# Optimization experiments

Measured on AMD Instinct MI355X. Metric: run time of the kernel, lower is better.

The kernel has to match this reference:

```python
import jax, jax.numpy as jnp
import numpy as np

N_EMBED = 1024
HEAD_SIZE = 128
B, T = 8, 2048


def setup_inputs() -> dict:
    key = jax.random.key(0)
    kx, kk, kq, kv = jax.random.split(key, 4)
    x = jax.random.normal(kx, (B, T, N_EMBED), dtype=jnp.float32)
    Wk = jax.random.normal(kk, (N_EMBED, HEAD_SIZE), dtype=jnp.float32) * (N_EMBED ** -0.5)
    Wq = jax.random.normal(kq, (N_EMBED, HEAD_SIZE), dtype=jnp.float32) * (N_EMBED ** -0.5)
    Wv = jax.random.normal(kv, (N_EMBED, HEAD_SIZE), dtype=jnp.float32) * (N_EMBED ** -0.5)
    return {"x": x, "Wk": Wk, "Wq": Wq, "Wv": Wv}


def reference(x, Wk, Wq, Wv):
    # x: [B, T, C]; single-head causal attention, dropout rate 0 (identity)
    t = x.shape[1]
    k = jnp.einsum("btc,ch->bth", x, Wk)  # keys
    q = jnp.einsum("btc,ch->bth", x, Wq)  # queries
    v = jnp.einsum("btc,ch->bth", x, Wv)  # values
    scale = k.shape[-1] ** -0.5
    scores = jnp.einsum("bqh,bkh->bqk", q, k) * scale  # [B, T, T]
    causal = jnp.tril(jnp.ones((t, t), dtype=bool))
    scores = jnp.where(causal, scores, -jnp.inf)
    attn = jax.nn.softmax(scores, axis=-1)
    return jnp.einsum("bqk,bkh->bqh", attn, v)
```

## Files before the change

kernel.cpp:

```cpp
#include <hip/hip_runtime.h>
#include <hip/hip_bf16.h>
#include <math.h>

#define B_ 8
#define T_ 2048
#define C_ 1024
#define D_ 128
#define M_ (B_*T_)

typedef __attribute__((ext_vector_type(8))) short short8;
typedef __attribute__((ext_vector_type(4))) float floatx4;
typedef __hip_bfloat16 bf16;

#define QSCALE 0.12751744416218247f

__global__ __launch_bounds__(256) void cvt_w2_kernel(const float* __restrict__ Wq,
                                                     const float* __restrict__ Wk,
                                                     const float* __restrict__ Wv,
                                                     bf16* __restrict__ Wt) {
    __shared__ bf16 tl[64][136];
    const int t = threadIdx.x;
    const int k0 = blockIdx.x * 64, g = blockIdx.y;
    const float* W = (g == 0) ? Wq : (g == 1) ? Wk : Wv;
    {
        int k = t >> 2, n0 = (t & 3) * 32;
        const float* src = W + (size_t)(k0 + k) * 128 + n0;
#pragma unroll
        for (int j = 0; j < 4; ++j) {
            float4 v0 = *(const float4*)(src + j * 8);
            float4 v1 = *(const float4*)(src + j * 8 + 4);
            union { short8 s; __hip_bfloat162 h[4]; } u;
            __hip_bfloat162 h;
            h.x = __float2bfloat16(v0.x); h.y = __float2bfloat16(v0.y); u.h[0] = h;
            h.x = __float2bfloat16(v0.z); h.y = __float2bfloat16(v0.w); u.h[1] = h;
            h.x = __float2bfloat16(v1.x); h.y = __float2bfloat16(v1.y); u.h[2] = h;
            h.x = __float2bfloat16(v1.z); h.y = __float2bfloat16(v1.w); u.h[3] = h;
            *(short8*)&tl[k][n0 + j * 8] = u.s;
        }
    }
    __syncthreads();
    {
        int n = t >> 1, ko = (t & 1) * 32;
        union { short8 s[4]; bf16 e[32]; } u;
#pragma unroll
        for (int i = 0; i < 32; ++i) u.e[i] = tl[ko + i][n];
        bf16* dst = Wt + (size_t)g * 131072 + (size_t)n * 1024 + k0 + ko;
#pragma unroll
        for (int j = 0; j < 4; ++j) *(short8*)(dst + j * 8) = u.s[j];
    }
}

__global__ __launch_bounds__(512, 2) void proj5_kernel(const float* __restrict__ x,
                                                       const bf16* __restrict__ Wt,
                                                       bf16* __restrict__ Qb,
                                                       bf16* __restrict__ Kb,
                                                       bf16* __restrict__ Vt) {
    __shared__ bf16 la[64][72];
    __shared__ bf16 lb[384][72];
    const int t = threadIdx.x;
    const int wave = t >> 6, lane = t & 63;
    const int quad = lane >> 4, l15 = lane & 15;
    const int wr2 = wave >> 2, wc2 = wave & 3;
    const int row0 = blockIdx.x * 64;
    const int ar = t >> 3, ao = (t & 7) * 8;

    floatx4 acc[2][6];
#pragma unroll
    for (int m = 0; m < 2; ++m)
#pragma unroll
        for (int n = 0; n < 6; ++n) acc[m][n] = (floatx4)0.0f;

    float4 xr0, xr1;
    short8 wreg[6];
    {
        const float* src = x + (size_t)(row0 + ar) * 1024 + ao;
        xr0 = *(const float4*)src;
        xr1 = *(const float4*)(src + 4);
#pragma unroll
        for (int j = 0; j < 6; ++j) {
            int c = t + j * 512;
            int rb = c >> 3, ob = (c & 7) * 8;
            wreg[j] = *(const short8*)(Wt + (size_t)rb * 1024 + ob);
        }
    }

    for (int kc = 0; kc < 16; ++kc) {
        __syncthreads();
        {
            union { short8 s; __hip_bfloat162 h[4]; } u;
            __hip_bfloat162 h;
            h.x = __float2bfloat16(xr0.x); h.y = __float2bfloat16(xr0.y); u.h[0] = h;
            h.x = __float2bfloat16(xr0.z); h.y = __float2bfloat16(xr0.w); u.h[1] = h;
            h.x = __float2bfloat16(xr1.x); h.y = __float2bfloat16(xr1.y); u.h[2] = h;
            h.x = __float2bfloat16(xr1.z); h.y = __float2bfloat16(xr1.w); u.h[3] = h;
            *(short8*)&la[ar][ao] = u.s;
        }
#pragma unroll
        for (int j = 0; j < 6; ++j) {
            int c = t + j * 512;
            int rb = c >> 3, ob = (c & 7) * 8;
            *(short8*)&lb[rb][ob] = wreg[j];
        }
        if (kc < 15) {
            const float* src = x + (size_t)(row0 + ar) * 1024 + (kc + 1) * 64 + ao;
            xr0 = *(const float4*)src;
            xr1 = *(const float4*)(src + 4);
#pragma unroll
            for (int j = 0; j < 6; ++j) {
                int c = t + j * 512;
                int rb = c >> 3, ob = (c & 7) * 8;
                wreg[j] = *(const short8*)(Wt + (size_t)rb * 1024 + (kc + 1) * 64 + ob);
            }
        }
        __syncthreads();
#pragma unroll
        for (int dk = 0; dk < 2; ++dk) {
            short8 af[2], bff[6];
#pragma unroll
            for (int m = 0; m < 2; ++m) af[m] = *(const short8*)&la[wr2 * 32 + m * 16 + l15][dk * 32 + quad * 8];
#pragma unroll
            for (int n = 0; n < 6; ++n) bff[n] = *(const short8*)&lb[wc2 * 96 + n * 16 + l15][dk * 32 + quad * 8];
#pragma unroll
            for (int m = 0; m < 2; ++m)
#pragma unroll
                for (int n = 0; n < 6; ++n)
                    acc[m][n] = __builtin_amdgcn_mfma_f32_16x16x32_bf16(af[m], bff[n], acc[m][n], 0, 0, 0);
        }
    }

    __syncthreads();
    bf16* vtl = &lb[0][0];
#pragma unroll
    for (int m = 0; m < 2; ++m)
#pragma unroll
        for (int r = 0; r < 4; ++r) {
            const int tt = wr2 * 32 + m * 16 + quad * 4 + r;
            const int row = row0 + tt;
#pragma unroll
            for (int n = 0; n < 6; ++n) {
                const int colb = wc2 * 96 + n * 16;
                const int g = colb >> 7;
                const int lc = (colb & 127) + l15;
                const float v = acc[m][n][r];
                if (g == 0)      Qb[(size_t)row * 128 + lc] = __float2bfloat16(v * QSCALE);
                else if (g == 1) Kb[(size_t)row * 128 + lc] = __float2bfloat16(v);
                else             vtl[tt * 136 + lc] = __float2bfloat16(v);
            }
        }
    __syncthreads();
    {
        int d = t >> 2, toff = (t & 3) * 16;
        union { short8 s[2]; bf16 e[16]; } u;
#pragma unroll
        for (int i = 0; i < 16; ++i) u.e[i] = vtl[(toff + i) * 136 + d];
        int bb = row0 >> 11, t0 = row0 & 2047;
        bf16* dst = Vt + (size_t)(bb * D_ + d) * T_ + t0 + toff;
        *(short8*)(dst)     = u.s[0];
        *(short8*)(dst + 8) = u.s[1];
    }
}

__global__ __launch_bounds__(256, 3) void flash_fm2_kernel(const bf16* __restrict__ Qb,
                                                           const bf16* __restrict__ Kb,
                                                           const bf16* __restrict__ Vt,
                                                           float* __restrict__ out,
                                                           bf16* __restrict__ Opart,
                                                           float* __restrict__ Lpart) {
    const int tile = blockIdx.x, seg = blockIdx.y, b = blockIdx.z;
    const int keys_total = (tile + 1) * 64;
    const int nseg = (keys_total + 255) >> 8;
    if (seg >= nseg) return;

    __shared__ bf16 lds_k[64][136];
    __shared__ bf16 lds_v[128][72];
    __shared__ bf16 lds_p[4][16][72];
    const int t = threadIdx.x;
    const int wave = t >> 6, lane = t & 63;
    const int quad = lane >> 4, l15 = lane & 15;
    const int q0 = tile * 64;
    const int k_start = seg << 8;
    const int k_end = min(k_start + 256, keys_total);
    const int nch = (k_end - k_start) >> 6;

    short8 qf[4];
    {
        int qm = q0 + wave * 16 + l15;
#pragma unroll
        for (int dk = 0; dk < 4; ++dk)
            qf[dk] = *(const short8*)(Qb + (size_t)(b * T_ + qm) * 128 + dk * 32 + quad * 8);
    }

    short8 kreg[4], vreg[4];
    {
        const int k0 = k_start;
#pragma unroll
        for (int j = 0; j < 4; ++j) {
            int c = t + j * 256;
            { int r = c >> 4, co = (c & 15) * 8;
              kreg[j] = *(const short8*)(Kb + (size_t)(b * T_ + k0 + r) * 128 + co); }
            { int d = c >> 3, co = (c & 7) * 8;
              vreg[j] = *(const short8*)(Vt + (size_t)b * (D_ * T_) + d * T_ + k0 + co); }
        }
    }

    floatx4 o_acc[8];
#pragma unroll
    for (int i = 0; i < 8; ++i) o_acc[i] = (floatx4)0.0f;
    float lp[4] = {0.f, 0.f, 0.f, 0.f};
    const int qrow = q0 + wave * 16 + quad * 4;

    for (int ch = 0; ch < nch; ++ch) {
        const int k0 = k_start + (ch << 6);
        __syncthreads();
#pragma unroll
        for (int j = 0; j < 4; ++j) {
            int c = t + j * 256;
            { int r = c >> 4, co = (c & 15) * 8; *(short8*)&lds_k[r][co] = kreg[j]; }
            { int d = c >> 3, co = (c & 7) * 8;  *(short8*)&lds_v[d][co] = vreg[j]; }
        }
        if (ch + 1 < nch) {
            const int kn = k0 + 64;
#pragma unroll
            for (int j = 0; j < 4; ++j) {
                int c = t + j * 256;
                { int r = c >> 4, co = (c & 15) * 8;
                  kreg[j] = *(const short8*)(Kb + (size_t)(b * T_ + kn + r) * 128 + co); }
                { int d = c >> 3, co = (c & 7) * 8;
                  vreg[j] = *(const short8*)(Vt + (size_t)b * (D_ * T_) + d * T_ + kn + co); }
            }
        }
        __syncthreads();

        floatx4 s[4];
#pragma unroll
        for (int nt = 0; nt < 4; ++nt) s[nt] = (floatx4)0.0f;
#pragma unroll
        for (int dk = 0; dk < 4; ++dk)
#pragma unroll
            for (int nt = 0; nt < 4; ++nt) {
                short8 kb = *(const short8*)&lds_k[nt * 16 + l15][dk * 32 + quad * 8];
                s[nt] = __builtin_amdgcn_mfma_f32_16x16x32_bf16(qf[dk], kb, s[nt], 0, 0, 0);
            }

        float sv[4][4];
#pragma unroll
        for (int nt = 0; nt < 4; ++nt)
#pragma unroll
            for (int r = 0; r < 4; ++r) sv[nt][r] = s[nt][r];

        if (k0 + 63 > q0) {
#pragma unroll
            for (int nt = 0; nt < 4; ++nt) {
                int key = k0 + nt * 16 + l15;
#pragma unroll
                for (int r = 0; r < 4; ++r)
                    if (key > qrow + r) sv[nt][r] = -1e30f;
            }
        }

#pragma unroll
        for (int nt = 0; nt < 4; ++nt)
#pragma unroll
            for (int r = 0; r < 4; ++r) sv[nt][r] = exp2f(sv[nt][r]);
#pragma unroll
        for (int r = 0; r < 4; ++r)
            lp[r] += (sv[0][r] + sv[1][r]) + (sv[2][r] + sv[3][r]);

#pragma unroll
        for (int nt = 0; nt < 4; ++nt)
#pragma unroll
            for (int r = 0; r < 4; ++r)
                lds_p[wave][quad * 4 + r][nt * 16 + l15] = __float2bfloat16(sv[nt][r]);
        short8 pa0 = *(const short8*)&lds_p[wave][l15][quad * 8];
        short8 pa1 = *(const short8*)&lds_p[wave][l15][32 + quad * 8];

#pragma unroll
        for (int nt = 0; nt < 8; ++nt) {
            short8 vb0 = *(const short8*)&lds_v[nt * 16 + l15][quad * 8];
            short8 vb1 = *(const short8*)&lds_v[nt * 16 + l15][32 + quad * 8];
            o_acc[nt] = __builtin_amdgcn_mfma_f32_16x16x32_bf16(pa0, vb0, o_acc[nt], 0, 0, 0);
            o_acc[nt] = __builtin_amdgcn_mfma_f32_16x16x32_bf16(pa1, vb1, o_acc[nt], 0, 0, 0);
        }
    }

    float l_i[4];
#pragma unroll
    for (int r = 0; r < 4; ++r) {
        float v = lp[r];
        v += __shfl_xor(v, 1);
        v += __shfl_xor(v, 2);
        v += __shfl_xor(v, 4);
        v += __shfl_xor(v, 8);
        l_i[r] = v;
    }

    const int lrow = wave * 16 + quad * 4;
    if (nseg == 1) {
        float inv_l[4];
#pragma unroll
        for (int r = 0; r < 4; ++r) inv_l[r] = 1.0f / l_i[r];
#pragma unroll
        for (int f = 0; f < 8; ++f)
#pragma unroll
            for (int r = 0; r < 4; ++r)
                out[(size_t)(b * T_ + qrow + r) * 128 + f * 16 + l15] = o_acc[f][r] * inv_l[r];
    } else {
        int pre = 0;
        for (int u = 4; u < tile; ++u) pre += (u + 4) >> 2;
        const size_t slot = (size_t)b * 140 + pre + seg;
        bf16* ob = Opart + slot * (64 * 128);
#pragma unroll
        for (int f = 0; f < 8; ++f)
#pragma unroll
            for (int r = 0; r < 4; ++r)
                ob[(size_t)(lrow + r) * 128 + f * 16 + l15] = __float2bfloat16(o_acc[f][r]);
        if (l15 == 0) {
#pragma unroll
            for (int r = 0; r < 4; ++r)
                Lpart[slot * 64 + lrow + r] = l_i[r];
        }
    }
}

__global__ __launch_bounds__(256) void combine4_kernel(const bf16* __restrict__ Opart,
                                                       const float* __restrict__ Lpart,
                                                       float* __restrict__ out) {
    const int tile = blockIdx.x + 4, b = blockIdx.y;
    const int nseg = (tile + 4) >> 2;
    int pre = 0;
    for (int u = 4; u < tile; ++u) pre += (u + 4) >> 2;
    const size_t slot0 = (size_t)b * 140 + pre;
    const int t = threadIdx.x;
    const int row = t >> 2, c0 = (t & 3) * 32;

    float lsum = 0.f;
    for (int j = 0; j < nseg; ++j) lsum += Lpart[(slot0 + j) * 64 + row];

    float acc[32];
#pragma unroll
    for (int i = 0; i < 32; ++i) acc[i] = 0.f;
    for (int j = 0; j < nseg; ++j) {
        const bf16* src = Opart + (slot0 + j) * (64 * 128) + (size_t)row * 128 + c0;
#pragma unroll
        for (int u = 0; u < 4; ++u) {
            short8 v8 = *(const short8*)(src + u * 8);
#pragma unroll
            for (int e = 0; e < 8; ++e) {
                union { unsigned int u32; float f; } cv;
                cv.u32 = ((unsigned int)(unsigned short)v8[e]) << 16;
                acc[u * 8 + e] += cv.f;
            }
        }
    }
    float inv = 1.0f / lsum;
    float* dst = out + (size_t)(b * T_ + tile * 64 + row) * 128 + c0;
#pragma unroll
    for (int i = 0; i < 32; ++i) dst[i] = acc[i] * inv;
}

extern "C" void kernel_launch(void* const* d_in, const int* in_sizes, int n_in,
                              void* d_out, int out_size, void* d_ws, size_t ws_size,
                              hipStream_t stream) {
    const float* x  = (const float*)d_in[0];
    const float* Wk = (const float*)d_in[1];
    const float* Wq = (const float*)d_in[2];
    const float* Wv = (const float*)d_in[3];
    float* out = (float*)d_out;

    char* ws = (char*)d_ws;
    bf16*  Wt    = (bf16*)ws;
    bf16*  Qb    = (bf16*)(ws + 786432);
    bf16*  Kb    = (bf16*)(ws + 4980736);
    bf16*  Vt    = (bf16*)(ws + 9175040);
    bf16*  Opart = (bf16*)(ws + 13369344);
    float* Lpart = (float*)(ws + 31719424);

    cvt_w2_kernel<<<dim3(16, 3), 256, 0, stream>>>(Wq, Wk, Wv, Wt);
    proj5_kernel<<<256, 512, 0, stream>>>(x, Wt, Qb, Kb, Vt);
    flash_fm2_kernel<<<dim3(32, 8, B_), 256, 0, stream>>>(Qb, Kb, Vt, out, Opart, Lpart);
    combine4_kernel<<<dim3(28, B_), 256, 0, stream>>>(Opart, Lpart, out);
}
```

Measured before the change: 82.16 us.

## Load projection MFMA operands directly from global memory, bypassing LDS staging

The projection kernel no longer stages x and W tiles through shared memory. Each lane loads its MFMA fragments straight from global memory into registers: x is prefetched one chunk ahead, and the weight fragments are loaded just before use. This removes two barriers per k-step and the LDS round trip, but it adds redundant global and L2 traffic, since the four waves that share x rows and the two waves that share W columns each fetch their own copy. The V transpose buffer also gets a 137 padding stride to reduce bank conflicts.

```diff
diff --git a/kernel.cpp b/kernel.cpp
--- a/kernel.cpp
+++ b/kernel.cpp
@@ -50,19 +50,20 @@
     }
 }
 
-__global__ __launch_bounds__(512, 2) void proj5_kernel(const float* __restrict__ x,
+__global__ __launch_bounds__(512, 2) void proj9_kernel(const float* __restrict__ x,
                                                        const bf16* __restrict__ Wt,
                                                        bf16* __restrict__ Qb,
                                                        bf16* __restrict__ Kb,
                                                        bf16* __restrict__ Vt) {
-    __shared__ bf16 la[64][72];
-    __shared__ bf16 lb[384][72];
+    __shared__ bf16 vtl[64 * 137];
     const int t = threadIdx.x;
     const int wave = t >> 6, lane = t & 63;
     const int quad = lane >> 4, l15 = lane & 15;
     const int wr2 = wave >> 2, wc2 = wave & 3;
     const int row0 = blockIdx.x * 64;
-    const int ar = t >> 3, ao = (t & 7) * 8;
+
+    const float* xb = x + (size_t)(row0 + wr2 * 32 + l15) * 1024 + quad * 8;
+    const bf16*  wb = Wt + (size_t)(wc2 * 96 + l15) * 1024 + quad * 8;
 
     floatx4 acc[2][6];
 #pragma unroll
@@ -70,66 +71,57 @@
 #pragma unroll
         for (int n = 0; n < 6; ++n) acc[m][n] = (floatx4)0.0f;
 
-    float4 xr0, xr1;
-    short8 wreg[6];
-    {
-        const float* src = x + (size_t)(row0 + ar) * 1024 + ao;
-        xr0 = *(const float4*)src;
-        xr1 = *(const float4*)(src + 4);
-#pragma unroll
-        for (int j = 0; j < 6; ++j) {
-            int c = t + j * 512;
-            int rb = c >> 3, ob = (c & 7) * 8;
-            wreg[j] = *(const short8*)(Wt + (size_t)rb * 1024 + ob);
-        }
-    }
+    float4 xp[8];
+#pragma unroll
+    for (int m = 0; m < 2; ++m)
+#pragma unroll
+        for (int dk = 0; dk < 2; ++dk) {
+            const float* s = xb + (size_t)m * 16384 + dk * 32;
+            xp[m * 4 + dk * 2 + 0] = *(const float4*)s;
+            xp[m * 4 + dk * 2 + 1] = *(const float4*)(s + 4);
+        }
 
     for (int kc = 0; kc < 16; ++kc) {
-        __syncthreads();
+        short8 af[2][2];
+#pragma unroll
+        for (int m = 0; m < 2; ++m)
+#pragma unroll
+            for (int dk = 0; dk < 2; ++dk) {
+                float4 a0 = xp[m * 4 + dk * 2 + 0];
+                float4 a1 = xp[m * 4 + dk * 2 + 1];
+                union { short8 s; __hip_bfloat162 h[4]; } u;
+                __hip_bfloat162 h;
+                h.x = __float2bfloat16(a0.x); h.y = __float2bfloat16(a0.y); u.h[0] = h;
+                h.x = __float2bfloat16(a0.z); h.y = __float2bfloat16(a0.w); u.h[1] = h;
+                h.x = __float2bfloat16(a1.x); h.y = __float2bfloat16(a1.y); u.h[2] = h;
+                h.x = __float2bfloat16(a1.z); h.y = __float2bfloat16(a1.w); u.h[3] = h;
+                af[m][dk] = u.s;
+            }
         {
-            union { short8 s; __hip_bfloat162 h[4]; } u;
-            __hip_bfloat162 h;
-            h.x = __float2bfloat16(xr0.x); h.y = __float2bfloat16(xr0.y); u.h[0] = h;
-            h.x = __float2bfloat16(xr0.z); h.y = __float2bfloat16(xr0.w); u.h[1] = h;
-            h.x = __float2bfloat16(xr1.x); h.y = __float2bfloat16(xr1.y); u.h[2] = h;
-            h.x = __float2bfloat16(xr1.z); h.y = __float2bfloat16(xr1.w); u.h[3] = h;
-            *(short8*)&la[ar][ao] = u.s;
-        }
-#pragma unroll
-        for (int j = 0; j < 6; ++j) {
-            int c = t + j * 512;
-            int rb = c >> 3, ob = (c & 7) * 8;
-            *(short8*)&lb[rb][ob] = wreg[j];
-        }
-        if (kc < 15) {
-            const float* src = x + (size_t)(row0 + ar) * 1024 + (kc + 1) * 64 + ao;
-            xr0 = *(const float4*)src;
-            xr1 = *(const float4*)(src + 4);
-#pragma unroll
-            for (int j = 0; j < 6; ++j) {
-                int c = t + j * 512;
-                int rb = c >> 3, ob = (c & 7) * 8;
-                wreg[j] = *(const short8*)(Wt + (size_t)rb * 1024 + (kc + 1) * 64 + ob);
-            }
-        }
-        __syncthreads();
+            const int kn = (kc + 1) & 15;
+#pragma unroll
+            for (int m = 0; m < 2; ++m)
+#pragma unroll
+                for (int dk = 0; dk < 2; ++dk) {
+                    const float* s = xb + (size_t)m * 16384 + kn * 64 + dk * 32;
+                    xp[m * 4 + dk * 2 + 0] = *(const float4*)s;
+                    xp[m * 4 + dk * 2 + 1] = *(const float4*)(s + 4);
+                }
+        }
 #pragma unroll
         for (int dk = 0; dk < 2; ++dk) {
-            short8 af[2], bff[6];
-#pragma unroll
-            for (int m = 0; m < 2; ++m) af[m] = *(const short8*)&la[wr2 * 32 + m * 16 + l15][dk * 32 + quad * 8];
-#pragma unroll
-            for (int n = 0; n < 6; ++n) bff[n] = *(const short8*)&lb[wc2 * 96 + n * 16 + l15][dk * 32 + quad * 8];
+            short8 bff[6];
+#pragma unroll
+            for (int n = 0; n < 6; ++n)
+                bff[n] = *(const short8*)(wb + (size_t)n * 16384 + kc * 64 + dk * 32);
 #pragma unroll
             for (int m = 0; m < 2; ++m)
 #pragma unroll
                 for (int n = 0; n < 6; ++n)
-                    acc[m][n] = __builtin_amdgcn_mfma_f32_16x16x32_bf16(af[m], bff[n], acc[m][n], 0, 0, 0);
-        }
-    }
-
-    __syncthreads();
-    bf16* vtl = &lb[0][0];
+                    acc[m][n] = __builtin_amdgcn_mfma_f32_16x16x32_bf16(af[m][dk], bff[n], acc[m][n], 0, 0, 0);
+        }
+    }
+
 #pragma unroll
     for (int m = 0; m < 2; ++m)
 #pragma unroll
@@ -144,7 +136,7 @@
                 const float v = acc[m][n][r];
                 if (g == 0)      Qb[(size_t)row * 128 + lc] = __float2bfloat16(v * QSCALE);
                 else if (g == 1) Kb[(size_t)row * 128 + lc] = __float2bfloat16(v);
-                else             vtl[tt * 136 + lc] = __float2bfloat16(v);
+                else             vtl[tt * 137 + lc] = __float2bfloat16(v);
             }
         }
     __syncthreads();
@@ -152,10 +144,10 @@
         int d = t >> 2, toff = (t & 3) * 16;
         union { short8 s[2]; bf16 e[16]; } u;
 #pragma unroll
-        for (int i = 0; i < 16; ++i) u.e[i] = vtl[(toff + i) * 136 + d];
+        for (int i = 0; i < 16; ++i) u.e[i] = vtl[(toff + i) * 137 + d];
         int bb = row0 >> 11, t0 = row0 & 2047;
         bf16* dst = Vt + (size_t)(bb * D_ + d) * T_ + t0 + toff;
-        *(short8*)(dst)     = u.s[0];
+        *(short8*)dst       = u.s[0];
         *(short8*)(dst + 8) = u.s[1];
     }
 }
@@ -376,7 +368,7 @@
     float* Lpart = (float*)(ws + 31719424);
 
     cvt_w2_kernel<<<dim3(16, 3), 256, 0, stream>>>(Wq, Wk, Wv, Wt);
-    proj5_kernel<<<256, 512, 0, stream>>>(x, Wt, Qb, Kb, Vt);
+    proj9_kernel<<<256, 512, 0, stream>>>(x, Wt, Qb, Kb, Vt);
     flash_fm2_kernel<<<dim3(32, 8, B_), 256, 0, stream>>>(Qb, Kb, Vt, out, Opart, Lpart);
     combine4_kernel<<<dim3(28, B_), 256, 0, stream>>>(Opart, Lpart, out);
 }
```

After: 132.3 us. 1.61x slower.

## Pre-swizzle weights into MFMA fragment order and stream them from registers

Applied to the files above, without the earlier changes.

The weight conversion kernel now writes W directly in MFMA B-fragment order, so the projection kernel loads B operands straight from global memory into registers and no longer stages them through LDS. Only the x tile goes through LDS, now double-buffered, which drops one barrier per k-step. Each wave computes a 64x48 output slice instead of 32x96, and the V transpose buffer uses a stride of 137 to reduce bank conflicts. The cost is more global loads per wave with less reuse of A, plus reliance on L2 for the weight fragments.

```diff
diff --git a/kernel.cpp b/kernel.cpp
--- a/kernel.cpp
+++ b/kernel.cpp
@@ -14,13 +14,14 @@
 
 #define QSCALE 0.12751744416218247f
 
-__global__ __launch_bounds__(256) void cvt_w2_kernel(const float* __restrict__ Wq,
+__global__ __launch_bounds__(256) void cvt_w3_kernel(const float* __restrict__ Wq,
                                                      const float* __restrict__ Wk,
                                                      const float* __restrict__ Wv,
-                                                     bf16* __restrict__ Wt) {
+                                                     bf16* __restrict__ Wt2) {
     __shared__ bf16 tl[64][136];
     const int t = threadIdx.x;
-    const int k0 = blockIdx.x * 64, g = blockIdx.y;
+    const int kc = blockIdx.x, g = blockIdx.y;
+    const int k0 = kc * 64;
     const float* W = (g == 0) ? Wq : (g == 1) ? Wk : Wv;
     {
         int k = t >> 2, n0 = (t & 3) * 32;
@@ -40,111 +41,121 @@
     }
     __syncthreads();
     {
-        int n = t >> 1, ko = (t & 1) * 32;
-        union { short8 s[4]; bf16 e[32]; } u;
-#pragma unroll
-        for (int i = 0; i < 32; ++i) u.e[i] = tl[ko + i][n];
-        bf16* dst = Wt + (size_t)g * 131072 + (size_t)n * 1024 + k0 + ko;
-#pragma unroll
-        for (int j = 0; j < 4; ++j) *(short8*)(dst + j * 8) = u.s[j];
-    }
-}
-
-__global__ __launch_bounds__(512, 2) void proj5_kernel(const float* __restrict__ x,
-                                                       const bf16* __restrict__ Wt,
-                                                       bf16* __restrict__ Qb,
-                                                       bf16* __restrict__ Kb,
-                                                       bf16* __restrict__ Vt) {
-    __shared__ bf16 la[64][72];
-    __shared__ bf16 lb[384][72];
+#pragma unroll
+        for (int j = 0; j < 4; ++j) {
+            int cid = t + j * 256;
+            int lane = cid & 63, dk = (cid >> 6) & 1, cb = cid >> 7;
+            int krow = dk * 32 + (lane >> 4) * 8;
+            int ncol = cb * 16 + (lane & 15);
+            union { short8 s; bf16 e[8]; } u;
+#pragma unroll
+            for (int e = 0; e < 8; ++e) u.e[e] = tl[krow + e][ncol];
+            bf16* dst = Wt2 + ((((size_t)(g * 8 + cb) * 16 + kc) * 2 + dk) * 64 + lane) * 8;
+            *(short8*)dst = u.s;
+        }
+    }
+}
+
+__global__ __launch_bounds__(512, 2) void proj10_kernel(const float* __restrict__ x,
+                                                        const bf16* __restrict__ Wt2,
+                                                        bf16* __restrict__ Qb,
+                                                        bf16* __restrict__ Kb,
+                                                        bf16* __restrict__ Vt) {
+    __shared__ bf16 smem[2 * 64 * 72];
     const int t = threadIdx.x;
     const int wave = t >> 6, lane = t & 63;
     const int quad = lane >> 4, l15 = lane & 15;
-    const int wr2 = wave >> 2, wc2 = wave & 3;
     const int row0 = blockIdx.x * 64;
-    const int ar = t >> 3, ao = (t & 7) * 8;
-
-    floatx4 acc[2][6];
-#pragma unroll
-    for (int m = 0; m < 2; ++m)
-#pragma unroll
-        for (int n = 0; n < 6; ++n) acc[m][n] = (floatx4)0.0f;
+    const int xrow = t >> 3, xc8 = (t & 7) * 8;
+    const float* xbase = x + (size_t)(row0 + xrow) * 1024 + xc8;
+    const bf16* wbase = Wt2 + (size_t)lane * 8;
+
+    floatx4 acc[4][3];
+#pragma unroll
+    for (int m = 0; m < 4; ++m)
+#pragma unroll
+        for (int n = 0; n < 3; ++n) acc[m][n] = (floatx4)0.0f;
 
     float4 xr0, xr1;
-    short8 wreg[6];
-    {
-        const float* src = x + (size_t)(row0 + ar) * 1024 + ao;
-        xr0 = *(const float4*)src;
-        xr1 = *(const float4*)(src + 4);
-#pragma unroll
-        for (int j = 0; j < 6; ++j) {
-            int c = t + j * 512;
-            int rb = c >> 3, ob = (c & 7) * 8;
-            wreg[j] = *(const short8*)(Wt + (size_t)rb * 1024 + ob);
-        }
-    }
+    short8 br[6];
+
+    xr0 = *(const float4*)xbase;
+    xr1 = *(const float4*)(xbase + 4);
+    {
+        union { short8 s; __hip_bfloat162 h[4]; } u;
+        __hip_bfloat162 h;
+        h.x = __float2bfloat16(xr0.x); h.y = __float2bfloat16(xr0.y); u.h[0] = h;
+        h.x = __float2bfloat16(xr0.z); h.y = __float2bfloat16(xr0.w); u.h[1] = h;
+        h.x = __float2bfloat16(xr1.x); h.y = __float2bfloat16(xr1.y); u.h[2] = h;
+        h.x = __float2bfloat16(xr1.z); h.y = __float2bfloat16(xr1.w); u.h[3] = h;
+        *(short8*)&smem[xrow * 72 + xc8] = u.s;
+    }
+    xr0 = *(const float4*)(xbase + 64);
+    xr1 = *(const float4*)(xbase + 68);
+#pragma unroll
+    for (int n = 0; n < 3; ++n)
+#pragma unroll
+        for (int dk = 0; dk < 2; ++dk)
+            br[dk * 3 + n] = *(const short8*)(wbase + ((size_t)((wave * 3 + n) * 16 + 0) * 1024 + dk * 512));
 
     for (int kc = 0; kc < 16; ++kc) {
         __syncthreads();
-        {
+        short8 brn[6];
+        if (kc < 15) {
+#pragma unroll
+            for (int n = 0; n < 3; ++n)
+#pragma unroll
+                for (int dk = 0; dk < 2; ++dk)
+                    brn[dk * 3 + n] = *(const short8*)(wbase + ((size_t)((wave * 3 + n) * 16 + kc + 1) * 1024 + dk * 512));
             union { short8 s; __hip_bfloat162 h[4]; } u;
             __hip_bfloat162 h;
             h.x = __float2bfloat16(xr0.x); h.y = __float2bfloat16(xr0.y); u.h[0] = h;
             h.x = __float2bfloat16(xr0.z); h.y = __float2bfloat16(xr0.w); u.h[1] = h;
             h.x = __float2bfloat16(xr1.x); h.y = __float2bfloat16(xr1.y); u.h[2] = h;
             h.x = __float2bfloat16(xr1.z); h.y = __float2bfloat16(xr1.w); u.h[3] = h;
-            *(short8*)&la[ar][ao] = u.s;
-        }
-#pragma unroll
-        for (int j = 0; j < 6; ++j) {
-            int c = t + j * 512;
-            int rb = c >> 3, ob = (c & 7) * 8;
-            *(short8*)&lb[rb][ob] = wreg[j];
+            *(short8*)&smem[((kc + 1) & 1) * 4608 + xrow * 72 + xc8] = u.s;
+        }
+        if (kc < 14) {
+            const float* s = xbase + (kc + 2) * 64;
+            xr0 = *(const float4*)s;
+            xr1 = *(const float4*)(s + 4);
+        }
+        const bf16* lc = smem + (kc & 1) * 4608;
+#pragma unroll
+        for (int dk = 0; dk < 2; ++dk) {
+            short8 af[4];
+#pragma unroll
+            for (int m = 0; m < 4; ++m)
+                af[m] = *(const short8*)&lc[(m * 16 + l15) * 72 + dk * 32 + quad * 8];
+#pragma unroll
+            for (int m = 0; m < 4; ++m)
+#pragma unroll
+                for (int n = 0; n < 3; ++n)
+                    acc[m][n] = __builtin_amdgcn_mfma_f32_16x16x32_bf16(af[m], br[dk * 3 + n], acc[m][n], 0, 0, 0);
         }
         if (kc < 15) {
-            const float* src = x + (size_t)(row0 + ar) * 1024 + (kc + 1) * 64 + ao;
-            xr0 = *(const float4*)src;
-            xr1 = *(const float4*)(src + 4);
-#pragma unroll
-            for (int j = 0; j < 6; ++j) {
-                int c = t + j * 512;
-                int rb = c >> 3, ob = (c & 7) * 8;
-                wreg[j] = *(const short8*)(Wt + (size_t)rb * 1024 + (kc + 1) * 64 + ob);
-            }
-        }
-        __syncthreads();
-#pragma unroll
-        for (int dk = 0; dk < 2; ++dk) {
-            short8 af[2], bff[6];
-#pragma unroll
-            for (int m = 0; m < 2; ++m) af[m] = *(const short8*)&la[wr2 * 32 + m * 16 + l15][dk * 32 + quad * 8];
-#pragma unroll
-            for (int n = 0; n < 6; ++n) bff[n] = *(const short8*)&lb[wc2 * 96 + n * 16 + l15][dk * 32 + quad * 8];
-#pragma unroll
-            for (int m = 0; m < 2; ++m)
-#pragma unroll
-                for (int n = 0; n < 6; ++n)
-                    acc[m][n] = __builtin_amdgcn_mfma_f32_16x16x32_bf16(af[m], bff[n], acc[m][n], 0, 0, 0);
+#pragma unroll
+            for (int i = 0; i < 6; ++i) br[i] = brn[i];
         }
     }
 
     __syncthreads();
-    bf16* vtl = &lb[0][0];
-#pragma unroll
-    for (int m = 0; m < 2; ++m)
+    bf16* vtl = smem;
+#pragma unroll
+    for (int m = 0; m < 4; ++m)
 #pragma unroll
         for (int r = 0; r < 4; ++r) {
-            const int tt = wr2 * 32 + m * 16 + quad * 4 + r;
+            const int tt = m * 16 + quad * 4 + r;
             const int row = row0 + tt;
 #pragma unroll
-            for (int n = 0; n < 6; ++n) {
-                const int colb = wc2 * 96 + n * 16;
+            for (int n = 0; n < 3; ++n) {
+                const int colb = wave * 48 + n * 16;
                 const int g = colb >> 7;
-                const int lc = (colb & 127) + l15;
+                const int lc_ = (colb & 127) + l15;
                 const float v = acc[m][n][r];
-                if (g == 0)      Qb[(size_t)row * 128 + lc] = __float2bfloat16(v * QSCALE);
-                else if (g == 1) Kb[(size_t)row * 128 + lc] = __float2bfloat16(v);
-                else             vtl[tt * 136 + lc] = __float2bfloat16(v);
+                if (g == 0)      Qb[(size_t)row * 128 + lc_] = __float2bfloat16(v * QSCALE);
+                else if (g == 1) Kb[(size_t)row * 128 + lc_] = __float2bfloat16(v);
+                else             vtl[tt * 137 + lc_] = __float2bfloat16(v);
             }
         }
     __syncthreads();
@@ -152,10 +163,10 @@
         int d = t >> 2, toff = (t & 3) * 16;
         union { short8 s[2]; bf16 e[16]; } u;
 #pragma unroll
-        for (int i = 0; i < 16; ++i) u.e[i] = vtl[(toff + i) * 136 + d];
+        for (int i = 0; i < 16; ++i) u.e[i] = vtl[(toff + i) * 137 + d];
         int bb = row0 >> 11, t0 = row0 & 2047;
         bf16* dst = Vt + (size_t)(bb * D_ + d) * T_ + t0 + toff;
-        *(short8*)(dst)     = u.s[0];
+        *(short8*)dst       = u.s[0];
         *(short8*)(dst + 8) = u.s[1];
     }
 }
@@ -368,15 +379,15 @@
     float* out = (float*)d_out;
 
     char* ws = (char*)d_ws;
-    bf16*  Wt    = (bf16*)ws;
+    bf16*  Wt2   = (bf16*)ws;
     bf16*  Qb    = (bf16*)(ws + 786432);
     bf16*  Kb    = (bf16*)(ws + 4980736);
     bf16*  Vt    = (bf16*)(ws + 9175040);
     bf16*  Opart = (bf16*)(ws + 13369344);
     float* Lpart = (float*)(ws + 31719424);
 
-    cvt_w2_kernel<<<dim3(16, 3), 256, 0, stream>>>(Wq, Wk, Wv, Wt);
-    proj5_kernel<<<256, 512, 0, stream>>>(x, Wt, Qb, Kb, Vt);
+    cvt_w3_kernel<<<dim3(16, 3), 256, 0, stream>>>(Wq, Wk, Wv, Wt2);
+    proj10_kernel<<<256, 512, 0, stream>>>(x, Wt2, Qb, Kb, Vt);
     flash_fm2_kernel<<<dim3(32, 8, B_), 256, 0, stream>>>(Qb, Kb, Vt, out, Opart, Lpart);
     combine4_kernel<<<dim3(28, B_), 256, 0, stream>>>(Opart, Lpart, out);
 }
```

Result: no change. 81.51 us (-0.8%).
